# Kernel tuning notes

Measured on AMD Instinct MI355X. Metric: run time of the kernel, lower is better.

## Reference

```python
import jax, jax.numpy as jnp
import numpy as np

B, L = 2, 2048          # batch, seq len (self-attention: M == L)
H, D, NB = 8, 16, 8     # n_heads, clifford_dim, n_blades (2^3 for sig_g=[1,1,1])
DM = H * D * NB         # d_model = 1024

# reverse() signs per blade for a 3D algebra, blade grades [0,1,1,1,2,2,2,3]:
# (-1)^{k(k-1)/2}; Euclidean metric signs from get_blade_signs are all +1,
# so the combined twist q_w = reverse(q) * signs is just these per-blade signs.
REV_SIGNS = jnp.array([1., 1., 1., 1., -1., -1., -1., -1.], dtype=jnp.float32)


def setup_inputs() -> dict:
    key = jax.random.key(0)
    ks = jax.random.split(key, 7)
    s = 1.0 / np.sqrt(DM)
    return {
        "query": jax.random.normal(ks[0], (B, L, DM), dtype=jnp.float32),
        "Wq": jax.random.normal(ks[1], (DM, DM), dtype=jnp.float32) * s,
        "bq": jax.random.normal(ks[2], (DM,), dtype=jnp.float32) * s,
        "Wk": jax.random.normal(ks[3], (DM, DM), dtype=jnp.float32) * s,
        "bk": jax.random.normal(ks[4], (DM,), dtype=jnp.float32) * s,
        "Wv": jax.random.normal(ks[5], (DM, DM), dtype=jnp.float32) * s,
        "bv": jax.random.normal(ks[6], (DM,), dtype=jnp.float32) * s,
    }


def reference(query, Wq, bq, Wk, bk, Wv, bv):
    b, l, _ = query.shape
    # projections (torch Linear: x @ W^T + b), reshape to (B,H,L,D,NB)
    def proj(x, W, bias):
        y = x @ W.T + bias
        return y.reshape(b, l, H, D, NB).transpose(0, 2, 1, 3, 4)

    q = proj(query, Wq, bq)
    k = proj(query, Wk, bk)   # self-attention: key = value = query
    v = proj(query, Wv, bv)

    q_w = q * REV_SIGNS  # reverse + blade-sign twist (elementwise over blade axis)
    scale = 1.0 / np.sqrt(D * NB)
    logits = jnp.einsum('bhldi,bhmdi->bhlm', q_w, k) * scale
    attn = jax.nn.softmax(logits, axis=-1)
    out = jnp.einsum('bhlm,bhmdi->bhldi', attn, v)
    out = out.transpose(0, 2, 1, 3, 4).reshape(b, l, -1)
    return out, attn.mean(axis=1)  # need_weights=True path
```

## Files before the change

kernel.cpp:

```cpp
#include <hip/hip_runtime.h>

typedef __attribute__((ext_vector_type(8))) __bf16 bf16x8;
typedef __attribute__((ext_vector_type(4))) __bf16 bf16x4;
typedef __attribute__((ext_vector_type(4))) float f32x4;
typedef __attribute__((ext_vector_type(16))) float f32x16;
typedef __attribute__((ext_vector_type(8))) unsigned short us8;
typedef __attribute__((ext_vector_type(4))) unsigned int u32x4;

constexpr float SCALE_L2E = 0.08838834764831845f * 1.4426950408889634f;

__device__ __forceinline__ unsigned short f2bf(float f) {
  unsigned int u = __float_as_uint(f);
  u = (u + 0x7FFFu + ((u >> 16) & 1u)) >> 16;
  return (unsigned short)u;
}

__device__ __forceinline__ void gl_lds16(const void* g, void* l) {
  __builtin_amdgcn_global_load_lds(
      (__attribute__((address_space(1))) void*)const_cast<void*>(g),
      (__attribute__((address_space(3))) void*)l, 16, 0, 0);
}

__global__ __launch_bounds__(256) void k_convert(
    const float* __restrict__ q, const float* __restrict__ wq,
    const float* __restrict__ wk, const float* __restrict__ wv,
    unsigned short* __restrict__ xb, unsigned short* __restrict__ wb) {
  long i = ((long)blockIdx.x * 256 + threadIdx.x) * 8;
  const float* s; unsigned short* d;
  if (i < 4194304)      { s = q  + i;             d = xb + i; }
  else if (i < 5242880) { s = wq + (i - 4194304); d = wb + (i - 4194304); }
  else if (i < 6291456) { s = wk + (i - 5242880); d = wb + 1048576 + (i - 5242880); }
  else                  { s = wv + (i - 6291456); d = wb + 2097152 + (i - 6291456); }
  float4 a = *(const float4*)s;
  float4 b = *(const float4*)(s + 4);
  us8 r;
  r[0]=f2bf(a.x); r[1]=f2bf(a.y); r[2]=f2bf(a.z); r[3]=f2bf(a.w);
  r[4]=f2bf(b.x); r[5]=f2bf(b.y); r[6]=f2bf(b.z); r[7]=f2bf(b.w);
  *(us8*)d = r;
}

__global__ __launch_bounds__(256) void k_proj(
    const unsigned short* __restrict__ xb, const unsigned short* __restrict__ wb,
    const float* __restrict__ bq, const float* __restrict__ bk, const float* __restrict__ bv,
    unsigned short* __restrict__ oq, unsigned short* __restrict__ ok_, unsigned short* __restrict__ vt) {
  __shared__ unsigned short As[4096];
  __shared__ unsigned short Bs[4096];
  const int t = threadIdx.x;
  const int wave = t >> 6, lane = t & 63;
  const int lrow = lane & 15, grp = lane >> 4;
  const int z = blockIdx.z;
  const unsigned short* w = wb + (size_t)z * 1048576;
  const float* bias = (z == 0) ? bq : ((z == 1) ? bk : bv);

  const unsigned short* asrc = xb + ((size_t)(blockIdx.y * 128 + (t >> 2)) * 1024 + (t & 3) * 8);
  const unsigned short* bsrc = w  + ((size_t)(blockIdx.x * 128 + (t >> 2)) * 1024 + (t & 3) * 8);

  f32x4 acc[4][4] = {};
  for (int kt = 0; kt < 32; ++kt) {
    gl_lds16(asrc + kt*32,              &As[t*8]);
    gl_lds16(asrc + kt*32 + 64*1024,    &As[2048 + t*8]);
    gl_lds16(bsrc + kt*32,              &Bs[t*8]);
    gl_lds16(bsrc + kt*32 + 64*1024,    &Bs[2048 + t*8]);
    __syncthreads();
    const int wr = wave >> 1, wc = wave & 1;
    bf16x8 af[4], bf[4];
#pragma unroll
    for (int mf = 0; mf < 4; ++mf)
      af[mf] = *(const bf16x8*)&As[(wr*64 + mf*16 + lrow)*32 + grp*8];
#pragma unroll
    for (int nf = 0; nf < 4; ++nf)
      bf[nf] = *(const bf16x8*)&Bs[(wc*64 + nf*16 + lrow)*32 + grp*8];
#pragma unroll
    for (int mf = 0; mf < 4; ++mf)
#pragma unroll
      for (int nf = 0; nf < 4; ++nf)
        acc[mf][nf] = __builtin_amdgcn_mfma_f32_16x16x32_bf16(af[mf], bf[nf], acc[mf][nf], 0, 0, 0);
    __syncthreads();
  }
  const int wr = wave >> 1, wc = wave & 1;
  if (z == 2) {
#pragma unroll
    for (int nf = 0; nf < 4; ++nf) {
      const int col = blockIdx.x*128 + wc*64 + nf*16 + lrow;
      const int h = col >> 7, dd = col & 127;
      const int dt = dd >> 5, lv = dd & 31;
      const float bsv = bias[col];
#pragma unroll
      for (int mf = 0; mf < 4; ++mf) {
        const int r0 = blockIdx.y*128 + wr*64 + mf*16 + grp*4;
        const int bb = r0 >> 11, m = r0 & 2047;
        const int mc = m >> 4, him = (m >> 3) & 1, j0 = m & 7;
        bf16x4 pv;
#pragma unroll
        for (int i = 0; i < 4; ++i) pv[i] = (__bf16)(acc[mf][nf][i] + bsv);
        const size_t off = ((((size_t)((bb*8 + h)*4 + dt))*128 + mc)*64 + lv + 32*him)*8 + j0;
        *(bf16x4*)&vt[off] = pv;
      }
    }
  } else {
    unsigned short* dst = (z == 0) ? oq : ok_;
    const float sign = (z == 0 && (lane & 7) >= 4) ? -1.0f : 1.0f;
#pragma unroll
    for (int nf = 0; nf < 4; ++nf) {
      const int col = blockIdx.x*128 + wc*64 + nf*16 + lrow;
      const float bsv = bias[col];
#pragma unroll
      for (int mf = 0; mf < 4; ++mf)
#pragma unroll
        for (int i = 0; i < 4; ++i) {
          const int row = blockIdx.y*128 + wr*64 + mf*16 + grp*4 + i;
          dst[(size_t)row*1024 + col] = f2bf((acc[mf][nf][i] + bsv) * sign);
        }
    }
  }
}

__global__ __launch_bounds__(256) void k_repack(const unsigned short* __restrict__ kws,
                                                unsigned short* __restrict__ kfrag) {
  const int c = blockIdx.x * 256 + threadIdx.x;
  const int lane = c & 63, kc = (c >> 6) & 7, mtile = (c >> 9) & 63, bh = c >> 15;
  const int b = bh >> 3, h = bh & 7;
  const int m = mtile*32 + (lane & 31);
  const int kd = kc*16 + (lane >> 5)*8;
  us8 v = *(const us8*)&kws[((size_t)(b*2048 + m))*1024 + h*128 + kd];
  *(us8*)&kfrag[(size_t)c * 8] = v;
}

__global__ __launch_bounds__(256) void k_attn_out(
    const unsigned short* __restrict__ qw, const unsigned short* __restrict__ kfrag,
    const unsigned short* __restrict__ vfrag, float* __restrict__ outp,
    float* __restrict__ rsw) {
  __shared__ __align__(16) char pool[65536];
  unsigned short (*KsL)[8192] = (unsigned short(*)[8192])pool;
  unsigned short (*VsL)[8192] = (unsigned short(*)[8192])(pool + 32768);
  float (*slab)[32][36] = (float(*)[32][36])pool;
  float (*rsred)[32] = (float(*)[32])(pool + 61440);
  float* invb = (float*)(pool + 62464);

  const int bid = blockIdx.x;
  const int xcd = bid & 7, r_ = bid >> 3;
  const int bh = (xcd << 1) | (r_ & 1);
  const int lt = r_ >> 1;
  const int b = bh >> 3, h = bh & 7;
  const int t = threadIdx.x;
  const int wave = t >> 6, lane = t & 63;
  const int mg = wave >> 1, lg = wave & 1;
  const int lm = lane & 31, hi = lane >> 5;

  bf16x8 qf[8];
  {
    const unsigned short* qp = qw + ((size_t)(b*2048 + lt*64 + lg*32 + lm))*1024
                                  + (size_t)h*128 + hi*8;
#pragma unroll
    for (int kc = 0; kc < 8; ++kc) qf[kc] = *(const bf16x8*)(qp + kc*16);
  }

  const unsigned short* kbp = kfrag + (size_t)bh*262144;
  const unsigned short* vbp = vfrag + (size_t)bh*262144;
  const int vdt = (t >> 6) & 3, vln = (t & 63) * 8;

  auto STAGE = [&](int buf, int it) {
#pragma unroll
    for (int q = 0; q < 2; ++q)
#pragma unroll
      for (int p = 0; p < 2; ++p)
        gl_lds16(kbp + (q*32 + it)*4096 + (p*256 + t)*8, &KsL[buf][q*4096 + (p*256 + t)*8]);
#pragma unroll
    for (int s = 0; s < 2; ++s)
#pragma unroll
      for (int w2 = 0; w2 < 2; ++w2)
        gl_lds16(vbp + vdt*65536 + (s*64 + it*2 + w2)*512 + vln,
                 &VsL[buf][s*4096 + w2*2048 + vdt*512 + vln]);
  };

  f32x16 oacc[4] = {};
  float rs = 0.f;

  STAGE(0, 0);
  __syncthreads();

  for (int it = 0; it < 32; ++it) {
    const int cur = it & 1;
    if (it + 1 < 32) STAGE(cur ^ 1, it + 1);

    bf16x8 kf[8];
#pragma unroll
    for (int kc = 0; kc < 8; ++kc)
      kf[kc] = *(const bf16x8*)&KsL[cur][mg*4096 + kc*512 + lane*8];
    f32x16 s = {};
#pragma unroll
    for (int kc = 0; kc < 8; ++kc)
      s = __builtin_amdgcn_mfma_f32_32x32x16_bf16(kf[kc], qf[kc], s, 0, 0, 0);

    bf16x8 vf[8];
#pragma unroll
    for (int w2 = 0; w2 < 2; ++w2)
#pragma unroll
      for (int dt = 0; dt < 4; ++dt)
        vf[w2*4 + dt] = *(const bf16x8*)&VsL[cur][mg*4096 + w2*2048 + dt*512 + lane*8];

    float e[16];
#pragma unroll
    for (int r = 0; r < 16; ++r) e[r] = __builtin_amdgcn_exp2f(s[r] * SCALE_L2E);
    float ps = 0.f;
#pragma unroll
    for (int r = 0; r < 16; ++r) ps += e[r];
    rs += ps;

    bf16x8 pf[2];
#pragma unroll
    for (int w2 = 0; w2 < 2; ++w2) {
      unsigned a0, a1, b0, b1;
      asm("v_cvt_pk_bf16_f32 %0, %1, %2" : "=v"(a0) : "v"(e[8*w2+0]), "v"(e[8*w2+1]));
      asm("v_cvt_pk_bf16_f32 %0, %1, %2" : "=v"(a1) : "v"(e[8*w2+2]), "v"(e[8*w2+3]));
      asm("v_cvt_pk_bf16_f32 %0, %1, %2" : "=v"(b0) : "v"(e[8*w2+4]), "v"(e[8*w2+5]));
      asm("v_cvt_pk_bf16_f32 %0, %1, %2" : "=v"(b1) : "v"(e[8*w2+6]), "v"(e[8*w2+7]));
      asm("v_permlane32_swap_b32 %0, %1" : "+v"(a0), "+v"(b0));
      asm("v_permlane32_swap_b32 %0, %1" : "+v"(a1), "+v"(b1));
      u32x4 pw = {a0, a1, b0, b1};
      pf[w2] = __builtin_bit_cast(bf16x8, pw);
    }

#pragma unroll
    for (int dt = 0; dt < 4; ++dt) {
      oacc[dt] = __builtin_amdgcn_mfma_f32_32x32x16_bf16(vf[dt],     pf[0], oacc[dt], 0, 0, 0);
      oacc[dt] = __builtin_amdgcn_mfma_f32_32x32x16_bf16(vf[4 + dt], pf[1], oacc[dt], 0, 0, 0);
    }
    __syncthreads();
  }

  rs += __shfl_xor(rs, 32, 64);
  if (lane < 32) rsred[wave][lm] = rs;
  __syncthreads();
  if (t < 64) {
    const int tlg = t >> 5, tl = t & 31;
    const float tot = rsred[tlg][tl] + rsred[2 + tlg][tl];
    rsw[(size_t)bh*2048 + lt*64 + t] = tot;
    invb[t] = 1.0f / tot;
  }

#pragma unroll
  for (int dt = 0; dt < 4; ++dt) {
    __syncthreads();
#pragma unroll
    for (int c = 0; c < 4; ++c) {
      float4 v4 = { oacc[dt][4*c + 0], oacc[dt][4*c + 1], oacc[dt][4*c + 2], oacc[dt][4*c + 3] };
      *(float4*)&slab[wave][lm][8*c + 4*hi] = v4;
    }
    __syncthreads();
    const int lgg = t >> 7, idx = t & 127;
    const int l = idx >> 2, d0 = (idx & 3) * 8;
    const float iv = invb[lgg*32 + l];
    float4 x0 = *(const float4*)&slab[lgg][l][d0];
    float4 x1 = *(const float4*)&slab[lgg][l][d0 + 4];
    float4 y0 = *(const float4*)&slab[2 + lgg][l][d0];
    float4 y1 = *(const float4*)&slab[2 + lgg][l][d0 + 4];
    float4 o0 = { (x0.x + y0.x)*iv, (x0.y + y0.y)*iv, (x0.z + y0.z)*iv, (x0.w + y0.w)*iv };
    float4 o1 = { (x1.x + y1.x)*iv, (x1.y + y1.y)*iv, (x1.z + y1.z)*iv, (x1.w + y1.w)*iv };
    float* op = outp + ((size_t)(b*2048 + lt*64 + lgg*32 + l))*1024 + h*128 + dt*32 + d0;
    *(float4*)op = o0;
    *(float4*)(op + 4) = o1;
  }
}

__global__ __launch_bounds__(512) void k_attn_mean(
    const unsigned short* __restrict__ qw, const unsigned short* __restrict__ kfrag,
    const float* __restrict__ rsw, float* __restrict__ meanp) {
  __shared__ unsigned short KsL[2][32768];
  __shared__ unsigned int slabu[8][32][18];
  __shared__ float inv_s[256];
  const int bid = blockIdx.x;
  const int xcd = bid & 7, lt = bid >> 3;
  const int b = xcd >> 2, ms = xcd & 3;
  const int t = threadIdx.x;
  const int h = t >> 6, lane = t & 63;
  const int lm = lane & 31, hi = lane >> 5;

  if (t < 256) inv_s[t] = 1.0f / rsw[(size_t)(b*8 + (t>>5))*2048 + lt*32 + (t&31)];

  bf16x8 qf[8];
  {
    const unsigned short* qp = qw + ((size_t)(b*2048 + lt*32 + lm))*1024 + h*128 + hi*8;
#pragma unroll
    for (int kc = 0; kc < 8; ++kc) qf[kc] = *(const bf16x8*)(qp + kc*16);
  }

  auto STAGE = [&](int buf, int it) {
#pragma unroll
    for (int i = 0; i < 8; ++i) {
      const int c = i*512 + t;
      const int hh = c >> 9;
      gl_lds16(kfrag + (size_t)(b*8 + hh)*262144 + (size_t)(ms*16 + it)*4096 + (c & 511)*8,
               &KsL[buf][c*8]);
    }
  };

  STAGE(0, 0);
  __syncthreads();

  float iv_r[16];
#pragma unroll
  for (int r = 0; r < 16; ++r)
    iv_r[r] = inv_s[h*32 + ((r & 3) + 8*(r >> 2) + 4*hi)];

  for (int it = 0; it < 16; ++it) {
    const int cur = it & 1;
    if (it + 1 < 16) STAGE(cur ^ 1, it + 1);

    bf16x8 kf[8];
#pragma unroll
    for (int kc = 0; kc < 8; ++kc)
      kf[kc] = *(const bf16x8*)&KsL[cur][(h*8 + kc)*512 + lane*8];
    f32x16 s = {};
#pragma unroll
    for (int kc = 0; kc < 8; ++kc)
      s = __builtin_amdgcn_mfma_f32_32x32x16_bf16(qf[kc], kf[kc], s, 0, 0, 0);

    float e[16];
#pragma unroll
    for (int r = 0; r < 16; ++r)
      e[r] = __builtin_amdgcn_exp2f(s[r] * SCALE_L2E) * iv_r[r];

#pragma unroll
    for (int gq = 0; gq < 4; ++gq) {
      unsigned p0, p1;
      asm("v_cvt_pk_bf16_f32 %0, %1, %2" : "=v"(p0) : "v"(e[gq*4+0]), "v"(e[gq*4+1]));
      asm("v_cvt_pk_bf16_f32 %0, %1, %2" : "=v"(p1) : "v"(e[gq*4+2]), "v"(e[gq*4+3]));
      uint2 w2; w2.x = p0; w2.y = p1;
      *(uint2*)&slabu[h][lm][gq*4 + hi*2] = w2;
    }
    __syncthreads();

    {
      const int m = t & 31, lp = t >> 5;
      float s0 = 0.f, s1 = 0.f;
#pragma unroll
      for (int w = 0; w < 8; ++w) {
        const unsigned pv = slabu[w][m][lp];
        s0 += __uint_as_float(pv << 16);
        s1 += __uint_as_float(pv & 0xFFFF0000u);
      }
      float* op = meanp + (size_t)(b*2048 + lt*32 + 2*lp)*2048 + (ms*16 + it)*32 + m;
      op[0]    = s0 * 0.125f;
      op[2048] = s1 * 0.125f;
    }
    __syncthreads();
  }
}

extern "C" void kernel_launch(void* const* d_in, const int* in_sizes, int n_in,
                              void* d_out, int out_size, void* d_ws, size_t ws_size,
                              hipStream_t stream) {
  (void)in_sizes; (void)n_in; (void)out_size; (void)ws_size;
  const float* query = (const float*)d_in[0];
  const float* Wq = (const float*)d_in[1];
  const float* bq = (const float*)d_in[2];
  const float* Wk = (const float*)d_in[3];
  const float* bk = (const float*)d_in[4];
  const float* Wv = (const float*)d_in[5];
  const float* bv = (const float*)d_in[6];
  float* outp  = (float*)d_out;
  float* meanp = outp + 4194304;

  char* ws = (char*)d_ws;
  unsigned short* xb    = (unsigned short*)(ws);
  unsigned short* wb    = (unsigned short*)(ws + 8388608);
  unsigned short* qws   = (unsigned short*)(ws + 14680064);
  unsigned short* kws   = (unsigned short*)(ws + 23068672);
  unsigned short* kfrag = (unsigned short*)(ws + 31457280);
  unsigned short* vfrag = (unsigned short*)(ws + 39845888);
  float*          rsw   = (float*)(ws + 48234496);

  k_convert<<<3584, 256, 0, stream>>>(query, Wq, Wk, Wv, xb, wb);
  k_proj<<<dim3(8, 32, 3), 256, 0, stream>>>(xb, wb, bq, bk, bv, qws, kws, vfrag);
  k_repack<<<2048, 256, 0, stream>>>(kws, kfrag);
  k_attn_out<<<512, 256, 0, stream>>>(qws, kfrag, vfrag, outp, rsw);
  k_attn_mean<<<512, 512, 0, stream>>>(qws, kfrag, rsw, meanp);
}
```

Measured before the change: 148.8 us.

## Process two query tiles per block in attn_mean to reuse staged K

```diff
diff --git a/kernel.cpp b/kernel.cpp
--- a/kernel.cpp
+++ b/kernel.cpp
@@ -263,12 +263,12 @@
   }
 }
 
-__global__ __launch_bounds__(512) void k_attn_mean(
+__global__ __launch_bounds__(512, 2) void k_attn_mean(
     const unsigned short* __restrict__ qw, const unsigned short* __restrict__ kfrag,
     const float* __restrict__ rsw, float* __restrict__ meanp) {
   __shared__ unsigned short KsL[2][32768];
   __shared__ unsigned int slabu[8][32][18];
-  __shared__ float inv_s[256];
+  __shared__ float inv_s[512];
   const int bid = blockIdx.x;
   const int xcd = bid & 7, lt = bid >> 3;
   const int b = xcd >> 2, ms = xcd & 3;
@@ -276,13 +276,16 @@
   const int h = t >> 6, lane = t & 63;
   const int lm = lane & 31, hi = lane >> 5;
 
-  if (t < 256) inv_s[t] = 1.0f / rsw[(size_t)(b*8 + (t>>5))*2048 + lt*32 + (t&31)];
-
-  bf16x8 qf[8];
+  inv_s[t] = 1.0f / rsw[(size_t)(b*8 + (t >> 6))*2048 + lt*64 + (t & 63)];
+
+  bf16x8 qf0[8], qf1[8];
   {
-    const unsigned short* qp = qw + ((size_t)(b*2048 + lt*32 + lm))*1024 + h*128 + hi*8;
-#pragma unroll
-    for (int kc = 0; kc < 8; ++kc) qf[kc] = *(const bf16x8*)(qp + kc*16);
+    const unsigned short* qp0 = qw + ((size_t)(b*2048 + lt*64 + lm))*1024 + h*128 + hi*8;
+#pragma unroll
+    for (int kc = 0; kc < 8; ++kc) qf0[kc] = *(const bf16x8*)(qp0 + kc*16);
+    const unsigned short* qp1 = qp0 + 32*1024;
+#pragma unroll
+    for (int kc = 0; kc < 8; ++kc) qf1[kc] = *(const bf16x8*)(qp1 + kc*16);
   }
 
   auto STAGE = [&](int buf, int it) {
@@ -298,10 +301,15 @@
   STAGE(0, 0);
   __syncthreads();
 
-  float iv_r[16];
-#pragma unroll
-  for (int r = 0; r < 16; ++r)
-    iv_r[r] = inv_s[h*32 + ((r & 3) + 8*(r >> 2) + 4*hi)];
+  float iv0[16], iv1[16];
+#pragma unroll
+  for (int r = 0; r < 16; ++r) {
+    const int lo = (r & 3) + 8*(r >> 2) + 4*hi;
+    iv0[r] = inv_s[h*64 + lo];
+    iv1[r] = inv_s[h*64 + 32 + lo];
+  }
+
+  const int rm = t & 31, lp = t >> 5;
 
   for (int it = 0; it < 16; ++it) {
     const int cur = it & 1;
@@ -311,40 +319,85 @@
 #pragma unroll
     for (int kc = 0; kc < 8; ++kc)
       kf[kc] = *(const bf16x8*)&KsL[cur][(h*8 + kc)*512 + lane*8];
-    f32x16 s = {};
-#pragma unroll
-    for (int kc = 0; kc < 8; ++kc)
-      s = __builtin_amdgcn_mfma_f32_32x32x16_bf16(qf[kc], kf[kc], s, 0, 0, 0);
-
-    float e[16];
-#pragma unroll
-    for (int r = 0; r < 16; ++r)
-      e[r] = __builtin_amdgcn_exp2f(s[r] * SCALE_L2E) * iv_r[r];
+
+    unsigned pk1[8];
+    {
+      f32x16 s = {};
+#pragma unroll
+      for (int kc = 0; kc < 8; ++kc)
+        s = __builtin_amdgcn_mfma_f32_32x32x16_bf16(qf0[kc], kf[kc], s, 0, 0, 0);
+#pragma unroll
+      for (int gq = 0; gq < 4; ++gq) {
+        float e0 = __builtin_amdgcn_exp2f(s[gq*4+0]*SCALE_L2E) * iv0[gq*4+0];
+        float e1 = __builtin_amdgcn_exp2f(s[gq*4+1]*SCALE_L2E) * iv0[gq*4+1];
+        float e2 = __builtin_amdgcn_exp2f(s[gq*4+2]*SCALE_L2E) * iv0[gq*4+2];
+        float e3 = __builtin_amdgcn_exp2f(s[gq*4+3]*SCALE_L2E) * iv0[gq*4+3];
+        unsigned p0, p1;
+        asm("v_cvt_pk_bf16_f32 %0, %1, %2" : "=v"(p0) : "v"(e0), "v"(e1));
+        asm("v_cvt_pk_bf16_f32 %0, %1, %2" : "=v"(p1) : "v"(e2), "v"(e3));
+        uint2 w2; w2.x = p0; w2.y = p1;
+        *(uint2*)&slabu[h][lm][gq*4 + hi*2] = w2;
+      }
+    }
+    asm volatile("s_waitcnt lgkmcnt(0)" ::: "memory");
+    __builtin_amdgcn_sched_barrier(0);
+    __builtin_amdgcn_s_barrier();
+
+    {
+      f32x16 s = {};
+#pragma unroll
+      for (int kc = 0; kc < 8; ++kc)
+        s = __builtin_amdgcn_mfma_f32_32x32x16_bf16(qf1[kc], kf[kc], s, 0, 0, 0);
+#pragma unroll
+      for (int gq = 0; gq < 4; ++gq) {
+        float e0 = __builtin_amdgcn_exp2f(s[gq*4+0]*SCALE_L2E) * iv1[gq*4+0];
+        float e1 = __builtin_amdgcn_exp2f(s[gq*4+1]*SCALE_L2E) * iv1[gq*4+1];
+        float e2 = __builtin_amdgcn_exp2f(s[gq*4+2]*SCALE_L2E) * iv1[gq*4+2];
+        float e3 = __builtin_amdgcn_exp2f(s[gq*4+3]*SCALE_L2E) * iv1[gq*4+3];
+        asm("v_cvt_pk_bf16_f32 %0, %1, %2" : "=v"(pk1[gq*2+0]) : "v"(e0), "v"(e1));
+        asm("v_cvt_pk_bf16_f32 %0, %1, %2" : "=v"(pk1[gq*2+1]) : "v"(e2), "v"(e3));
+      }
+    }
+    {
+      float a0 = 0.f, a1 = 0.f;
+#pragma unroll
+      for (int w = 0; w < 8; ++w) {
+        const unsigned pv = slabu[w][rm][lp];
+        a0 += __uint_as_float(pv << 16);
+        a1 += __uint_as_float(pv & 0xFFFF0000u);
+      }
+      float* op = meanp + (size_t)(b*2048 + lt*64 + 2*lp)*2048 + (ms*16 + it)*32 + rm;
+      op[0]    = a0 * 0.125f;
+      op[2048] = a1 * 0.125f;
+    }
+    asm volatile("s_waitcnt lgkmcnt(0)" ::: "memory");
+    __builtin_amdgcn_sched_barrier(0);
+    __builtin_amdgcn_s_barrier();
 
 #pragma unroll
     for (int gq = 0; gq < 4; ++gq) {
-      unsigned p0, p1;
-      asm("v_cvt_pk_bf16_f32 %0, %1, %2" : "=v"(p0) : "v"(e[gq*4+0]), "v"(e[gq*4+1]));
-      asm("v_cvt_pk_bf16_f32 %0, %1, %2" : "=v"(p1) : "v"(e[gq*4+2]), "v"(e[gq*4+3]));
-      uint2 w2; w2.x = p0; w2.y = p1;
+      uint2 w2; w2.x = pk1[gq*2+0]; w2.y = pk1[gq*2+1];
       *(uint2*)&slabu[h][lm][gq*4 + hi*2] = w2;
     }
-    __syncthreads();
+    asm volatile("s_waitcnt lgkmcnt(0)" ::: "memory");
+    __builtin_amdgcn_sched_barrier(0);
+    __builtin_amdgcn_s_barrier();
 
     {
-      const int m = t & 31, lp = t >> 5;
-      float s0 = 0.f, s1 = 0.f;
+      float a0 = 0.f, a1 = 0.f;
 #pragma unroll
       for (int w = 0; w < 8; ++w) {
-        const unsigned pv = slabu[w][m][lp];
-        s0 += __uint_as_float(pv << 16);
-        s1 += __uint_as_float(pv & 0xFFFF0000u);
+        const unsigned pv = slabu[w][rm][lp];
+        a0 += __uint_as_float(pv << 16);
+        a1 += __uint_as_float(pv & 0xFFFF0000u);
       }
-      float* op = meanp + (size_t)(b*2048 + lt*32 + 2*lp)*2048 + (ms*16 + it)*32 + m;
-      op[0]    = s0 * 0.125f;
-      op[2048] = s1 * 0.125f;
-    }
-    __syncthreads();
+      float* op = meanp + (size_t)(b*2048 + lt*64 + 32 + 2*lp)*2048 + (ms*16 + it)*32 + rm;
+      op[0]    = a0 * 0.125f;
+      op[2048] = a1 * 0.125f;
+    }
+    asm volatile("s_waitcnt vmcnt(0) lgkmcnt(0)" ::: "memory");
+    __builtin_amdgcn_sched_barrier(0);
+    __builtin_amdgcn_s_barrier();
   }
 }
 
@@ -375,5 +428,5 @@
   k_proj<<<dim3(8, 32, 3), 256, 0, stream>>>(xb, wb, bq, bk, bv, qws, kws, vfrag);
   k_repack<<<2048, 256, 0, stream>>>(kws, kfrag);
   k_attn_out<<<512, 256, 0, stream>>>(qws, kfrag, vfrag, outp, rsw);
-  k_attn_mean<<<512, 512, 0, stream>>>(qws, kfrag, rsw, meanp);
-}
+  k_attn_mean<<<256, 512, 0, stream>>>(qws, kfrag, rsw, meanp);
+}
```

Measured after the change: 137.1 us. 1.09x faster.
